# Kernel optimization log

Hardware: AMD Instinct MI355X
Metric: run time of the kernel (lower is better)

The kernel has to match this reference:

```python
import jax, jax.numpy as jnp
import numpy as np

COMMITMENT_COST = 0.25


def setup_inputs() -> dict:
    key = jax.random.key(0)
    k1, k2 = jax.random.split(key)
    B, D, H, W = 64, 64, 32, 32
    K = 512
    x = jax.random.normal(k1, (B, D, H, W), dtype=jnp.float32)
    # torch init: uniform_(-1/K, 1/K)
    codebook = jax.random.uniform(k2, (K, D), dtype=jnp.float32,
                                  minval=-1.0 / K, maxval=1.0 / K)
    return {"x": x, "codebook": codebook}


def reference(x, codebook):
    B, D, H, W = x.shape
    K = codebook.shape[0]
    in_re = jnp.transpose(x, (0, 2, 3, 1))          # [B,H,W,D]
    flat = in_re.reshape(-1, D)                      # [N,D], N=B*H*W
    dist = (jnp.sum(flat * flat, axis=1, keepdims=True)
            + jnp.sum(codebook * codebook, axis=1)
            - 2.0 * jnp.matmul(flat, codebook.T))    # [N,K]
    idx = jnp.argmin(dist, axis=1)                   # [N]
    encoding = jax.nn.one_hot(idx, K, dtype=jnp.float32)  # [N,K]
    softmax_histogram = jnp.sum(jax.nn.softmax(-dist, axis=-1).reshape(B, -1, K), axis=1)  # [B,K]
    quantized = jnp.matmul(encoding, codebook).reshape(in_re.shape)  # [B,H,W,D]
    e_latent_loss = jnp.mean((jax.lax.stop_gradient(quantized) - in_re) ** 2)
    q_latent_loss = jnp.mean((quantized - jax.lax.stop_gradient(in_re)) ** 2)
    loss = q_latent_loss + COMMITMENT_COST * e_latent_loss
    # straight-through estimator
    quant_st = in_re + jax.lax.stop_gradient(quantized - in_re)
    avg_probs = jnp.mean(encoding, axis=0)
    perplexity = jnp.exp(-jnp.sum(avg_probs * jnp.log(avg_probs + 1e-10)))
    quant_out = jnp.transpose(quant_st, (0, 3, 1, 2))  # back to NCHW
    encoding_indice = idx.reshape(B, -1)               # [B, H*W]
    # per-batch histogram of code usage == sum of one-hots over spatial dim
    index_program = jnp.sum(encoding.reshape(B, -1, K), axis=1)  # [B,K]
    return (quant_out, loss, perplexity, encoding_indice, index_program, softmax_histogram)
```

## Files before the change

kernel.cpp:

```cpp
#include <hip/hip_runtime.h>


#define OFF_LOSS 4194304
#define OFF_PERP 4194305
#define OFF_ENC  4194306
#define OFF_IP   4259842
#define OFF_SH   4292610

#define WS_CBT   0
#define WS_CE2   32768
#define WS_SHP   33280
#define WS_LOSS  557568
#define WS_CNT   561664


typedef float f16v __attribute__((ext_vector_type(16)));

typedef __attribute__((address_space(1))) const void g_void;
typedef __attribute__((address_space(3))) void lds_void;
#define GLOAD_LDS(G, S) \
    __builtin_amdgcn_global_load_lds((g_void*)(G), (lds_void*)(S), 16, 0, 0)

__global__ __launch_bounds__(256) void vq_prep(const float* __restrict__ cb,
                                               float* __restrict__ ws)
{
    if (blockIdx.x == 0 && threadIdx.x == 0)
        ((int*)ws)[WS_CNT] = 0;

    const int t  = blockIdx.x * 256 + threadIdx.x;
    const int kg = t >> 4;
    const int j  = t & 15;
    const float4 v = ((const float4*)cb)[(kg << 4) + j];
    float pr = v.x * v.x + v.y * v.y + v.z * v.z + v.w * v.w;
    #pragma unroll
    for (int off = 1; off < 16; off <<= 1) pr += __shfl_xor(pr, off, 16);
    if (j == 0) ws[WS_CE2 + kg] = pr;
    const int s  = ((kg >> 8) << 1) + (j >> 3);
    const int dl = (j << 2) & 31;
    float* base = ws + WS_CBT + (s << 13) + (dl << 8) + (kg & 255);
    base[0]   = v.x;
    base[256] = v.y;
    base[512] = v.z;
    base[768] = v.w;
}

#define FMA4(ACC, AV, K4) \
    ACC[(K4) + 0] = fmaf((AV), bq.x, ACC[(K4) + 0]); \
    ACC[(K4) + 1] = fmaf((AV), bq.y, ACC[(K4) + 1]); \
    ACC[(K4) + 2] = fmaf((AV), bq.z, ACC[(K4) + 2]); \
    ACC[(K4) + 3] = fmaf((AV), bq.w, ACC[(K4) + 3]);

#define STAGE_SEG(S) do { \
    GLOAD_LDS(&cbT4[((S) << 11) + t],        &csT4[t]); \
    GLOAD_LDS(&cbT4[((S) << 11) + 256 + t],  &csT4[256 + t]); \
    GLOAD_LDS(&cbT4[((S) << 11) + 512 + t],  &csT4[512 + t]); \
    GLOAD_LDS(&cbT4[((S) << 11) + 768 + t],  &csT4[768 + t]); \
    GLOAD_LDS(&cbT4[((S) << 11) + 1024 + t], &csT4[1024 + t]); \
    GLOAD_LDS(&cbT4[((S) << 11) + 1280 + t], &csT4[1280 + t]); \
    GLOAD_LDS(&cbT4[((S) << 11) + 1536 + t], &csT4[1536 + t]); \
    GLOAD_LDS(&cbT4[((S) << 11) + 1792 + t], &csT4[1792 + t]); \
} while (0)

#define GEMM_SEG(KC, H) do { \
    _Pragma("unroll 2") \
    for (int db = 0; db < 8; ++db) { \
        _Pragma("unroll") \
        for (int j = 0; j < 4; ++j) { \
            const int dl = (db << 2) + j; \
            const int d  = ((H) << 5) + dl; \
            const float4 a0 = *(const float4*)&xs[(d << 6) + (tr << 3)]; \
            const float4 a1 = *(const float4*)&xs[(d << 6) + (tr << 3) + 4]; \
            const float* cb0 = &csT[(dl << 8) + (tc << 2)]; \
            { \
                const float4 bq = *(const float4*)cb0; \
                FMA4(acc0, a0.x, (KC) << 3) \
                FMA4(acc1, a0.y, (KC) << 3) \
                FMA4(acc2, a0.z, (KC) << 3) \
                FMA4(acc3, a0.w, (KC) << 3) \
                FMA4(acc4, a1.x, (KC) << 3) \
                FMA4(acc5, a1.y, (KC) << 3) \
                FMA4(acc6, a1.z, (KC) << 3) \
                FMA4(acc7, a1.w, (KC) << 3) \
            } \
            { \
                const float4 bq = *(const float4*)(cb0 + 128); \
                FMA4(acc0, a0.x, ((KC) << 3) + 4) \
                FMA4(acc1, a0.y, ((KC) << 3) + 4) \
                FMA4(acc2, a0.z, ((KC) << 3) + 4) \
                FMA4(acc3, a0.w, ((KC) << 3) + 4) \
                FMA4(acc4, a1.x, ((KC) << 3) + 4) \
                FMA4(acc5, a1.y, ((KC) << 3) + 4) \
                FMA4(acc6, a1.z, ((KC) << 3) + 4) \
                FMA4(acc7, a1.w, ((KC) << 3) + 4) \
            } \
        } \
    } \
} while (0)

#define EPI_C(C, ACC) { \
    const int k = (((C) >> 2) << 7) + (tc << 2) + ((C) & 3); \
    const float t1 = xxr + ce2[k]; \
    const float dist = t1 - 2.f * ACC[C]; \
    ACC[C] = dist; \
    if (dist < m) { m = dist; bk = k; } }

#define EXP_C(C, ACC) { \
    const float e = __expf(m - ACC[C]); \
    ACC[C] = e; z += e; }

#define ROW_EPI(I, ACC, INVZ) do { \
    const int row = (tr << 3) + (I); \
    const float xxr = sxx[row]; \
    float m = 1e30f; int bk = 0; \
    EPI_C(0, ACC)  EPI_C(1, ACC)  EPI_C(2, ACC)  EPI_C(3, ACC) \
    EPI_C(4, ACC)  EPI_C(5, ACC)  EPI_C(6, ACC)  EPI_C(7, ACC) \
    EPI_C(8, ACC)  EPI_C(9, ACC)  EPI_C(10, ACC) EPI_C(11, ACC) \
    EPI_C(12, ACC) EPI_C(13, ACC) EPI_C(14, ACC) EPI_C(15, ACC) \
    _Pragma("unroll") \
    for (int off = 1; off < 32; off <<= 1) { \
        const float mo = __shfl_xor(m, off, 32); \
        const int   ko = __shfl_xor(bk, off, 32); \
        if (mo < m || (mo == m && ko < bk)) { m = mo; bk = ko; } \
    } \
    float z = 0.f; \
    EXP_C(0, ACC)  EXP_C(1, ACC)  EXP_C(2, ACC)  EXP_C(3, ACC) \
    EXP_C(4, ACC)  EXP_C(5, ACC)  EXP_C(6, ACC)  EXP_C(7, ACC) \
    EXP_C(8, ACC)  EXP_C(9, ACC)  EXP_C(10, ACC) EXP_C(11, ACC) \
    EXP_C(12, ACC) EXP_C(13, ACC) EXP_C(14, ACC) EXP_C(15, ACC) \
    _Pragma("unroll") \
    for (int off = 1; off < 32; off <<= 1) z += __shfl_xor(z, off, 32); \
    INVZ = 1.f / z; \
    if (tc == 0) { \
        sidx[row] = bk; \
        enc[((size_t)b << 10) + row0 + row] = (float)bk; \
    } \
} while (0)

#define HIST_C(C) { \
    const int k = (((C) >> 2) << 7) + (tc << 2) + ((C) & 3); \
    float cs = 0.f; \
    cs += acc0[C] * invz0; cs += acc1[C] * invz1; \
    cs += acc2[C] * invz2; cs += acc3[C] * invz3; \
    cs += acc4[C] * invz4; cs += acc5[C] * invz5; \
    cs += acc6[C] * invz6; cs += acc7[C] * invz7; \
    atomicAdd(&shist[k], cs); }

__global__ __launch_bounds__(256, 1) void vq_main(
    const float* __restrict__ x, const float* __restrict__ cb,
    const float* __restrict__ wsc,
    float* __restrict__ wso,
    float* __restrict__ out)
{
    __shared__ float  xs[64 * 64];
    __shared__ float  csT[32 * 256];
    __shared__ float  ce2[512];
    __shared__ float  sxx[64];
    __shared__ int    sidx[64];

    const int t    = threadIdx.x;
    const int blk  = blockIdx.x;
    const int b    = blk >> 4;
    const int row0 = (blk & 15) << 6;
    const int tr   = t >> 5;
    const int tc   = t & 31;

    const float4* cbT4 = (const float4*)(wsc + WS_CBT);
    float4* csT4 = (float4*)csT;

    {
        const float4* xb4 = (const float4*)(x + ((size_t)b << 16) + row0);
        #pragma unroll
        for (int p = 0; p < 4; ++p) {
            const int fi = (p << 8) + t;
            const int d  = fi >> 4;
            const int r4 = fi & 15;
            GLOAD_LDS(&xb4[(d << 8) + r4], &xs[(d << 6) + (r4 << 2)]);
        }
    }
    STAGE_SEG(0);
    if (t < 128) ((float4*)ce2)[t] = ((const float4*)(wsc + WS_CE2))[t];

    __syncthreads();

    if (t < 64) {
        float s = 0.f;
        for (int d = 0; d < 64; ++d) { const float v = xs[(d << 6) + t]; s = fmaf(v, v, s); }
        sxx[t] = s;
    }

    f16v acc0 = 0.f, acc1 = 0.f, acc2 = 0.f, acc3 = 0.f;
    f16v acc4 = 0.f, acc5 = 0.f, acc6 = 0.f, acc7 = 0.f;

    GEMM_SEG(0, 0);
    __syncthreads();
    STAGE_SEG(1);
    __syncthreads();
    GEMM_SEG(0, 1);
    __syncthreads();
    STAGE_SEG(2);
    __syncthreads();
    GEMM_SEG(1, 0);
    __syncthreads();
    STAGE_SEG(3);
    __syncthreads();
    GEMM_SEG(1, 1);

    float* enc = out + OFF_ENC;
    float invz0, invz1, invz2, invz3, invz4, invz5, invz6, invz7;
    ROW_EPI(0, acc0, invz0);
    ROW_EPI(1, acc1, invz1);
    ROW_EPI(2, acc2, invz2);
    ROW_EPI(3, acc3, invz3);
    ROW_EPI(4, acc4, invz4);
    ROW_EPI(5, acc5, invz5);
    ROW_EPI(6, acc6, invz6);
    ROW_EPI(7, acc7, invz7);

    __syncthreads();

    float* shist = csT;
    shist[t] = 0.f; shist[t + 256] = 0.f;
    __syncthreads();
    HIST_C(0)  HIST_C(1)  HIST_C(2)  HIST_C(3)
    HIST_C(4)  HIST_C(5)  HIST_C(6)  HIST_C(7)
    HIST_C(8)  HIST_C(9)  HIST_C(10) HIST_C(11)
    HIST_C(12) HIST_C(13) HIST_C(14) HIST_C(15)
    __syncthreads();
    {
        float* wsh = wso + WS_SHP + ((size_t)blk << 9);
        wsh[t]       = shist[t];
        wsh[t + 256] = shist[t + 256];
    }

    const int r4 = (t & 15) << 2;
    const int dq = t >> 4;
    const int c0 = sidx[r4], c1 = sidx[r4 + 1], c2 = sidx[r4 + 2], c3 = sidx[r4 + 3];
    float lsum = 0.f;
    #pragma unroll
    for (int p = 0; p < 4; ++p) {
        const int d = (p << 4) + dq;
        float4 q;
        q.x = cb[(c0 << 6) + d];
        q.y = cb[(c1 << 6) + d];
        q.z = cb[(c2 << 6) + d];
        q.w = cb[(c3 << 6) + d];
        const float4 xv = *(const float4*)&xs[(d << 6) + r4];
        const float d0 = q.x - xv.x, d1 = q.y - xv.y, d2 = q.z - xv.z, d3 = q.w - xv.w;
        lsum = fmaf(d0, d0, lsum); lsum = fmaf(d1, d1, lsum);
        lsum = fmaf(d2, d2, lsum); lsum = fmaf(d3, d3, lsum);
        *(float4*)&out[(((size_t)(b << 6) + d) << 10) + row0 + r4] = q;
    }
    #pragma unroll
    for (int off = 1; off < 64; off <<= 1) lsum += __shfl_xor(lsum, off, 64);
    if ((t & 63) == 0) wso[WS_LOSS + (blk << 2) + (t >> 6)] = lsum;
}

__global__ __launch_bounds__(512) void vq_tail(float* __restrict__ ws,
                                               float* __restrict__ out)
{
    __shared__ int hist[512];
    __shared__ int s_last;
    const int b = blockIdx.x, t = threadIdx.x;
    const float* p = ws + WS_SHP + ((size_t)b << 13) + t;
    float s = 0.f;
    #pragma unroll
    for (int j = 0; j < 16; ++j) s += p[j << 9];
    out[OFF_SH + (b << 9) + t] = s;
    hist[t] = 0;
    __syncthreads();
    const float* enc = out + OFF_ENC + ((size_t)b << 10);
    const int ca  = (int)enc[t];
    const int cbn = (int)enc[t + 512];
    atomicAdd(&hist[ca], 1);
    atomicAdd(&hist[cbn], 1);
    __syncthreads();
    out[OFF_IP + (b << 9) + t] = (float)hist[t];

    __threadfence();
    if (t == 0) s_last = (atomicAdd(&((int*)ws)[WS_CNT], 1) == 63);
    __syncthreads();
    if (!s_last) return;
    __threadfence();

    __shared__ float red[8], red2[8];
    const float* ip = out + OFF_IP;
    float c0 = 0.f, c1 = 0.f, c2 = 0.f, c3 = 0.f;
    #pragma unroll
    for (int bb = 0; bb < 64; bb += 4) {
        c0 += ip[((bb + 0) << 9) + t];
        c1 += ip[((bb + 1) << 9) + t];
        c2 += ip[((bb + 2) << 9) + t];
        c3 += ip[((bb + 3) << 9) + t];
    }
    const float c = (c0 + c1) + (c2 + c3);
    const float pav = c * (1.0f / 65536.f);
    float h = pav * logf(pav + 1e-10f);
    const float* wl = ws + WS_LOSS;
    float ls = 0.f;
    #pragma unroll
    for (int j = 0; j < 8; ++j) ls += wl[(j << 9) + t];
    #pragma unroll
    for (int off = 1; off < 64; off <<= 1) {
        h  += __shfl_xor(h, off, 64);
        ls += __shfl_xor(ls, off, 64);
    }
    if ((t & 63) == 0) { red[t >> 6] = h; red2[t >> 6] = ls; }
    __syncthreads();
    if (t == 0) {
        float H = 0.f, L = 0.f;
        #pragma unroll
        for (int w = 0; w < 8; ++w) { H += red[w]; L += red2[w]; }
        out[OFF_PERP] = expf(-H);
        out[OFF_LOSS] = L * (1.25f / 4194304.f);
    }
}

extern "C" void kernel_launch(void* const* d_in, const int* in_sizes, int n_in,
                              void* d_out, int out_size, void* d_ws, size_t ws_size,
                              hipStream_t stream)
{
    const float* x  = (const float*)d_in[0];
    const float* cb = (const float*)d_in[1];
    float* out = (float*)d_out;
    float* ws  = (float*)d_ws;
    (void)ws_size;

    vq_prep <<<32,   256, 0, stream>>>(cb, ws);
    vq_main <<<1024, 256, 0, stream>>>(x, cb, ws, ws, out);
    vq_tail <<<64,   512, 0, stream>>>(ws, out);
}
```

Measured before the change: 175.1 us.

## Stage codebook by D-slices across all 512 codes instead of K-halves

The transposed codebook is now laid out and staged in four 16-dimension slices that each cover all 512 codes, rather than 32-dimension slices over 256 codes. Each GEMM step therefore loads one row of x and feeds four codebook quads into all 16 accumulators per row, halving x LDS reads per FMA. The epilogue also reads the squared codebook norms as float4 instead of scalars. The number of stage/sync phases is unchanged, and register pressure from the unroll-4 inner loop may shift.

```diff
diff --git a/kernel.cpp b/kernel.cpp
--- a/kernel.cpp
+++ b/kernel.cpp
@@ -35,13 +35,13 @@
     #pragma unroll
     for (int off = 1; off < 16; off <<= 1) pr += __shfl_xor(pr, off, 16);
     if (j == 0) ws[WS_CE2 + kg] = pr;
-    const int s  = ((kg >> 8) << 1) + (j >> 3);
-    const int dl = (j << 2) & 31;
-    float* base = ws + WS_CBT + (s << 13) + (dl << 8) + (kg & 255);
-    base[0]   = v.x;
-    base[256] = v.y;
-    base[512] = v.z;
-    base[768] = v.w;
+    const int s   = j >> 2;
+    const int dl4 = (j & 3) << 2;
+    float* base = ws + WS_CBT + (s << 13) + (dl4 << 9) + kg;
+    base[0]    = v.x;
+    base[512]  = v.y;
+    base[1024] = v.z;
+    base[1536] = v.w;
 }
 
 #define FMA4(ACC, AV, K4) \
@@ -61,48 +61,45 @@
     GLOAD_LDS(&cbT4[((S) << 11) + 1792 + t], &csT4[1792 + t]); \
 } while (0)
 
-#define GEMM_SEG(KC, H) do { \
-    _Pragma("unroll 2") \
-    for (int db = 0; db < 8; ++db) { \
-        _Pragma("unroll") \
-        for (int j = 0; j < 4; ++j) { \
-            const int dl = (db << 2) + j; \
-            const int d  = ((H) << 5) + dl; \
-            const float4 a0 = *(const float4*)&xs[(d << 6) + (tr << 3)]; \
-            const float4 a1 = *(const float4*)&xs[(d << 6) + (tr << 3) + 4]; \
-            const float* cb0 = &csT[(dl << 8) + (tc << 2)]; \
-            { \
-                const float4 bq = *(const float4*)cb0; \
-                FMA4(acc0, a0.x, (KC) << 3) \
-                FMA4(acc1, a0.y, (KC) << 3) \
-                FMA4(acc2, a0.z, (KC) << 3) \
-                FMA4(acc3, a0.w, (KC) << 3) \
-                FMA4(acc4, a1.x, (KC) << 3) \
-                FMA4(acc5, a1.y, (KC) << 3) \
-                FMA4(acc6, a1.z, (KC) << 3) \
-                FMA4(acc7, a1.w, (KC) << 3) \
-            } \
-            { \
-                const float4 bq = *(const float4*)(cb0 + 128); \
-                FMA4(acc0, a0.x, ((KC) << 3) + 4) \
-                FMA4(acc1, a0.y, ((KC) << 3) + 4) \
-                FMA4(acc2, a0.z, ((KC) << 3) + 4) \
-                FMA4(acc3, a0.w, ((KC) << 3) + 4) \
-                FMA4(acc4, a1.x, ((KC) << 3) + 4) \
-                FMA4(acc5, a1.y, ((KC) << 3) + 4) \
-                FMA4(acc6, a1.z, ((KC) << 3) + 4) \
-                FMA4(acc7, a1.w, ((KC) << 3) + 4) \
-            } \
-        } \
+#define FMA_QUAD(Q, OFFS) do { \
+    const float4 bq = *(const float4*)(cb0 + (OFFS)); \
+    FMA4(acc0, a0.x, (Q) << 2) \
+    FMA4(acc1, a0.y, (Q) << 2) \
+    FMA4(acc2, a0.z, (Q) << 2) \
+    FMA4(acc3, a0.w, (Q) << 2) \
+    FMA4(acc4, a1.x, (Q) << 2) \
+    FMA4(acc5, a1.y, (Q) << 2) \
+    FMA4(acc6, a1.z, (Q) << 2) \
+    FMA4(acc7, a1.w, (Q) << 2) \
+} while (0)
+
+#define GEMM_SEG(S) do { \
+    _Pragma("unroll 4") \
+    for (int dl = 0; dl < 16; ++dl) { \
+        const int d = ((S) << 4) + dl; \
+        const float4 a0 = *(const float4*)&xs[(d << 6) + (tr << 3)]; \
+        const float4 a1 = *(const float4*)&xs[(d << 6) + (tr << 3) + 4]; \
+        const float* cb0 = &csT[(dl << 9) + (tc << 2)]; \
+        FMA_QUAD(0, 0); \
+        FMA_QUAD(1, 128); \
+        FMA_QUAD(2, 256); \
+        FMA_QUAD(3, 384); \
     } \
 } while (0)
 
-#define EPI_C(C, ACC) { \
+#define EPI_C(C, ACC, CE) { \
     const int k = (((C) >> 2) << 7) + (tc << 2) + ((C) & 3); \
-    const float t1 = xxr + ce2[k]; \
+    const float t1 = xxr + (CE); \
     const float dist = t1 - 2.f * ACC[C]; \
     ACC[C] = dist; \
     if (dist < m) { m = dist; bk = k; } }
+
+#define EPI_Q(Q, ACC) { \
+    const float4 cq = *(const float4*)&ce2[((Q) << 7) + (tc << 2)]; \
+    EPI_C(((Q) << 2) + 0, ACC, cq.x) \
+    EPI_C(((Q) << 2) + 1, ACC, cq.y) \
+    EPI_C(((Q) << 2) + 2, ACC, cq.z) \
+    EPI_C(((Q) << 2) + 3, ACC, cq.w) }
 
 #define EXP_C(C, ACC) { \
     const float e = __expf(m - ACC[C]); \
@@ -112,10 +109,7 @@
     const int row = (tr << 3) + (I); \
     const float xxr = sxx[row]; \
     float m = 1e30f; int bk = 0; \
-    EPI_C(0, ACC)  EPI_C(1, ACC)  EPI_C(2, ACC)  EPI_C(3, ACC) \
-    EPI_C(4, ACC)  EPI_C(5, ACC)  EPI_C(6, ACC)  EPI_C(7, ACC) \
-    EPI_C(8, ACC)  EPI_C(9, ACC)  EPI_C(10, ACC) EPI_C(11, ACC) \
-    EPI_C(12, ACC) EPI_C(13, ACC) EPI_C(14, ACC) EPI_C(15, ACC) \
+    EPI_Q(0, ACC)  EPI_Q(1, ACC)  EPI_Q(2, ACC)  EPI_Q(3, ACC) \
     _Pragma("unroll") \
     for (int off = 1; off < 32; off <<= 1) { \
         const float mo = __shfl_xor(m, off, 32); \
@@ -152,7 +146,7 @@
     float* __restrict__ out)
 {
     __shared__ float  xs[64 * 64];
-    __shared__ float  csT[32 * 256];
+    __shared__ float  csT[16 * 512];
     __shared__ float  ce2[512];
     __shared__ float  sxx[64];
     __shared__ int    sidx[64];
@@ -191,19 +185,19 @@
     f16v acc0 = 0.f, acc1 = 0.f, acc2 = 0.f, acc3 = 0.f;
     f16v acc4 = 0.f, acc5 = 0.f, acc6 = 0.f, acc7 = 0.f;
 
-    GEMM_SEG(0, 0);
+    GEMM_SEG(0);
     __syncthreads();
     STAGE_SEG(1);
     __syncthreads();
-    GEMM_SEG(0, 1);
+    GEMM_SEG(1);
     __syncthreads();
     STAGE_SEG(2);
     __syncthreads();
-    GEMM_SEG(1, 0);
+    GEMM_SEG(2);
     __syncthreads();
     STAGE_SEG(3);
     __syncthreads();
-    GEMM_SEG(1, 1);
+    GEMM_SEG(3);
 
     float* enc = out + OFF_ENC;
     float invz0, invz1, invz2, invz3, invz4, invz5, invz6, invz7;
```

After: 172.1 us. Within noise of the previous version (-1.7%).
